# Optimization experiments

Measured on AMD Instinct MI355X. Metric: run time of the kernel, lower is better.

The kernel has to match this reference:

```python
import jax, jax.numpy as jnp
import numpy as np

BN_EPS = 1e-5


def trilinear_sample(feat, grid):
    """F.grid_sample 5D, mode='bilinear', padding_mode='border', align_corners=True.
    feat: (B,C,D,H,W); grid: (B,N,3) in [-1,1], last dim ordered (x,y,z) -> (W,H,D).
    Returns (B,N,C)."""
    B, C, D, H, W = feat.shape
    # align_corners=True unnormalization; border padding == clamp continuous coord
    x = jnp.clip((grid[..., 0] + 1.0) * 0.5 * (W - 1), 0.0, W - 1)
    y = jnp.clip((grid[..., 1] + 1.0) * 0.5 * (H - 1), 0.0, H - 1)
    z = jnp.clip((grid[..., 2] + 1.0) * 0.5 * (D - 1), 0.0, D - 1)
    x0 = jnp.floor(x).astype(jnp.int32); x1 = jnp.minimum(x0 + 1, W - 1)
    y0 = jnp.floor(y).astype(jnp.int32); y1 = jnp.minimum(y0 + 1, H - 1)
    z0 = jnp.floor(z).astype(jnp.int32); z1 = jnp.minimum(z0 + 1, D - 1)
    wx = (x - x0)[:, None, :]  # (B,1,N)
    wy = (y - y0)[:, None, :]
    wz = (z - z0)[:, None, :]
    flat = feat.reshape(B, C, D * H * W)

    def gather(zi, yi, xi):
        idx = (zi * H + yi) * W + xi            # (B,N)
        return jnp.take_along_axis(flat, idx[:, None, :], axis=2)  # (B,C,N)

    c00 = gather(z0, y0, x0) * (1 - wx) + gather(z0, y0, x1) * wx
    c01 = gather(z0, y1, x0) * (1 - wx) + gather(z0, y1, x1) * wx
    c10 = gather(z1, y0, x0) * (1 - wx) + gather(z1, y0, x1) * wx
    c11 = gather(z1, y1, x0) * (1 - wx) + gather(z1, y1, x1) * wx
    c0 = c00 * (1 - wy) + c01 * wy
    c1 = c10 * (1 - wy) + c11 * wy
    out = c0 * (1 - wz) + c1 * wz               # (B,C,N)
    return out.transpose(0, 2, 1)                # (B,N,C)


def batchnorm(x, gamma, beta, mean, var):
    # inference-mode BatchNorm1d over channel (last) dim
    return (x - mean) * jax.lax.rsqrt(var + BN_EPS) * gamma + beta


def setup_inputs() -> dict:
    key = jax.random.key(0)
    ks = jax.random.split(key, 16)
    B, C, D, H, W = 2, 128, 64, 64, 64
    N = 65536
    h1, h2 = 512, 512
    inp = {
        "dense_features": jax.random.normal(ks[0], (B, C, D, H, W), dtype=jnp.float32),
        "query_points": jax.random.uniform(ks[1], (B, N, 3), dtype=jnp.float32),
        "W1": jax.random.normal(ks[2], (C, h1), dtype=jnp.float32) / np.sqrt(C),
        "b1": jax.random.normal(ks[3], (h1,), dtype=jnp.float32) * 0.01,
        "g1": jax.random.uniform(ks[4], (h1,), dtype=jnp.float32, minval=0.5, maxval=1.5),
        "be1": jax.random.normal(ks[5], (h1,), dtype=jnp.float32) * 0.1,
        "m1": jax.random.normal(ks[6], (h1,), dtype=jnp.float32) * 0.1,
        "v1": jax.random.uniform(ks[7], (h1,), dtype=jnp.float32, minval=0.5, maxval=1.5),
        "W2": jax.random.normal(ks[8], (h1, h2), dtype=jnp.float32) / np.sqrt(h1),
        "b2": jax.random.normal(ks[9], (h2,), dtype=jnp.float32) * 0.01,
        "g2": jax.random.uniform(ks[10], (h2,), dtype=jnp.float32, minval=0.5, maxval=1.5),
        "be2": jax.random.normal(ks[11], (h2,), dtype=jnp.float32) * 0.1,
        "m2": jax.random.normal(ks[12], (h2,), dtype=jnp.float32) * 0.1,
        "v2": jax.random.uniform(ks[13], (h2,), dtype=jnp.float32, minval=0.5, maxval=1.5),
        "W3": jax.random.normal(ks[14], (h2, 1), dtype=jnp.float32) / np.sqrt(h2),
        "b3": jax.random.normal(ks[15], (1,), dtype=jnp.float32) * 0.01,
    }
    return inp


def reference(dense_features, query_points, W1, b1, g1, be1, m1, v1,
              W2, b2, g2, be2, m2, v2, W3, b3):
    grid = 2.0 * query_points - 1.0                       # (B,N,3)
    feats = trilinear_sample(dense_features, grid)        # (B,N,128)
    h = jax.nn.relu(batchnorm(jnp.einsum('bnc,ch->bnh', feats, W1) + b1, g1, be1, m1, v1))
    h = jax.nn.relu(batchnorm(jnp.einsum('bnc,ch->bnh', h, W2) + b2, g2, be2, m2, v2))
    out = jnp.einsum('bnc,ch->bnh', h, W3) + b3           # (B,N,1)
    return out
```

## Files before the change

kernel.cpp:

```cpp
#include <hip/hip_runtime.h>
#include <hip/hip_bf16.h>

using bf16x8 = __attribute__((ext_vector_type(8))) short;
using f32x4  = __attribute__((ext_vector_type(4))) float;
using u32x4  = __attribute__((ext_vector_type(4))) unsigned int;
typedef unsigned short u16;
typedef unsigned int u32;

#define NB    2
#define NC    128
#define NPTS  65536
#define MTOT  (NB*NPTS)
#define NTILE (MTOT/64)

static __device__ __forceinline__ u16 f2bf(float f) {
    u32 u = __float_as_uint(f);
    u32 r = (u + 0x7FFFu + ((u >> 16) & 1u)) >> 16;
    return (u16)r;
}
static __device__ __forceinline__ float bflo(u32 d) { return __uint_as_float(d << 16); }
static __device__ __forceinline__ float bfhi(u32 d) { return __uint_as_float(d & 0xFFFF0000u); }

__global__ void prep_kernel(
    const float* __restrict__ W1, const float* __restrict__ W2,
    const float* __restrict__ b1, const float* __restrict__ g1, const float* __restrict__ be1,
    const float* __restrict__ m1, const float* __restrict__ v1,
    const float* __restrict__ b2, const float* __restrict__ g2, const float* __restrict__ be2,
    const float* __restrict__ m2, const float* __restrict__ v2,
    u16* __restrict__ W1p, u16* __restrict__ W2p,
    float* __restrict__ s1, float* __restrict__ t1,
    float* __restrict__ s2, float* __restrict__ t2)
{
    int id = blockIdx.x * 256 + threadIdx.x;
    {
        int l = id & 63, nf = (id >> 6) & 3, kk = (id >> 8) & 15, w = id >> 12;
        int n  = w * 64 + nf * 16 + (l & 15);
        int c0 = kk * 32 + (l >> 4) * 8;
        #pragma unroll
        for (int j = 0; j < 8; ++j)
            W2p[id * 8 + j] = f2bf(W2[(size_t)(c0 + j) * 512 + n]);
    }
    if (id < 8192) {
        int l = id & 63, nf = (id >> 6) & 3, kk = (id >> 8) & 3, w = id >> 10;
        int n  = w * 64 + nf * 16 + (l & 15);
        int c0 = kk * 32 + (l >> 4) * 8;
        #pragma unroll
        for (int j = 0; j < 8; ++j)
            W1p[id * 8 + j] = f2bf(W1[(size_t)(c0 + j) * 512 + n]);
    }
    if (id < 512) {
        float s = g1[id] * rsqrtf(v1[id] + 1e-5f);
        s1[id] = s;
        t1[id] = (b1[id] - m1[id]) * s + be1[id];
        float ss = g2[id] * rsqrtf(v2[id] + 1e-5f);
        s2[id] = ss;
        t2[id] = (b2[id] - m2[id]) * ss + be2[id];
    }
}

__global__ __launch_bounds__(256) void transpose_kernel(const float* __restrict__ feat,
                                                        u16* __restrict__ featT)
{
    __shared__ float tile[128][33];
    int blk = blockIdx.x;
    int b   = blk >> 13;
    int v0  = (blk & 8191) << 5;
    int t   = threadIdx.x;
    const float* fb = feat + ((size_t)b << 25) + v0;
    int c_l = t >> 3, f4 = t & 7;
    #pragma unroll
    for (int r = 0; r < 4; ++r) {
        int c = c_l + 32 * r;
        float4 v = *(const float4*)(fb + ((size_t)c << 18) + f4 * 4);
        tile[c][f4 * 4 + 0] = v.x;
        tile[c][f4 * 4 + 1] = v.y;
        tile[c][f4 * 4 + 2] = v.z;
        tile[c][f4 * 4 + 3] = v.w;
    }
    __syncthreads();
    u32* outp = (u32*)(featT + (((size_t)b << 18) + v0) * 128);
    #pragma unroll
    for (int r = 0; r < 2; ++r) {
        int idx = t + 256 * r;
        int v   = idx >> 4;
        int c4  = idx & 15;
        u32x4 o;
        #pragma unroll
        for (int k = 0; k < 4; ++k) {
            float lo = tile[8 * c4 + 2 * k + 0][v];
            float hi = tile[8 * c4 + 2 * k + 1][v];
            o[k] = (u32)f2bf(lo) | ((u32)f2bf(hi) << 16);
        }
        *(u32x4*)(outp + (size_t)v * 64 + c4 * 4) = o;
    }
}

template<bool SAMP>
__global__ __launch_bounds__(512, 4) void fused_kernel(
    const u16* __restrict__ featT, const u16* __restrict__ feats,
    const float* __restrict__ qp,
    const u16* __restrict__ W1p, const u16* __restrict__ W2p,
    const float* __restrict__ s1, const float* __restrict__ t1,
    const float* __restrict__ s2, const float* __restrict__ t2,
    const float* __restrict__ W3, const float* __restrict__ b3,
    float* __restrict__ out)
{
    __shared__ u16 h1[64 * 512];
    __shared__ float outb[512];
    u16* atile = h1;

    const int tidx = threadIdx.x;
    const int w    = tidx >> 6;
    const int l    = tidx & 63;
    const int l15  = l & 15;
    const int lq   = l >> 4;
    const int m0   = blockIdx.x * 64;
    const int n0   = w * 64;

    const u16* B1 = W1p + (size_t)(w * 4)  * 4 * 512;
    const u16* B2 = W2p + (size_t)(w * 16) * 4 * 512;

#define LOADB1(dst, kk) { _Pragma("unroll") for (int nf = 0; nf < 4; ++nf) \
    (dst)[nf] = *(const bf16x8*)(B1 + ((kk) * 4 + nf) * 512 + l * 8); }
#define LOADB2(dst, kk) { _Pragma("unroll") for (int nf = 0; nf < 4; ++nf) \
    (dst)[nf] = *(const bf16x8*)(B2 + ((kk) * 4 + nf) * 512 + l * 8); }
#define LDSA(dst, kk) { _Pragma("unroll") for (int mf = 0; mf < 4; ++mf) { \
    int row = mf * 16 + l15; \
    (dst)[mf] = *(const bf16x8*)(atile + row * 128 + ((((kk) * 4 + lq) ^ (row & 7)) << 3)); } }
#define LOADA2(dst, kk) { _Pragma("unroll") for (int mf = 0; mf < 4; ++mf) { \
    int row = mf * 16 + l15; \
    (dst)[mf] = *(const bf16x8*)(h1 + row * 512 + (((kk) * 32 + lq * 8) ^ ((row & 7) << 3))); } }

    if (SAMP) {
        const int li = tidx & 15;
        const int pr = tidx >> 4;
        const int co = li * 4;
        #pragma unroll
        for (int half = 0; half < 2; ++half) {
            int row = pr + 32 * half;
            int p   = m0 + row;
            int b   = p >> 16;
            float qx = qp[p * 3 + 0], qy = qp[p * 3 + 1], qz = qp[p * 3 + 2];
            float x = fminf(fmaxf(qx * 63.0f, 0.0f), 63.0f);
            float y = fminf(fmaxf(qy * 63.0f, 0.0f), 63.0f);
            float z = fminf(fmaxf(qz * 63.0f, 0.0f), 63.0f);
            int x0 = (int)floorf(x), y0 = (int)floorf(y), z0 = (int)floorf(z);
            int x1 = min(x0 + 1, 63), y1 = min(y0 + 1, 63), z1 = min(z0 + 1, 63);
            float wx = x - (float)x0, wy = y - (float)y0, wz = z - (float)z0;
            const u32* fb = (const u32*)featT + ((size_t)b << 24);
            int zy00 = z0 * 4096 + y0 * 64, zy01 = z0 * 4096 + y1 * 64;
            int zy10 = z1 * 4096 + y0 * 64, zy11 = z1 * 4096 + y1 * 64;
            u32x4 d000 = *(const u32x4*)(fb + (size_t)(zy00 + x0) * 64 + co);
            u32x4 d001 = *(const u32x4*)(fb + (size_t)(zy00 + x1) * 64 + co);
            u32x4 d010 = *(const u32x4*)(fb + (size_t)(zy01 + x0) * 64 + co);
            u32x4 d011 = *(const u32x4*)(fb + (size_t)(zy01 + x1) * 64 + co);
            u32x4 d100 = *(const u32x4*)(fb + (size_t)(zy10 + x0) * 64 + co);
            u32x4 d101 = *(const u32x4*)(fb + (size_t)(zy10 + x1) * 64 + co);
            u32x4 d110 = *(const u32x4*)(fb + (size_t)(zy11 + x0) * 64 + co);
            u32x4 d111 = *(const u32x4*)(fb + (size_t)(zy11 + x1) * 64 + co);
            float omx = 1.0f - wx, omy = 1.0f - wy, omz = 1.0f - wz;
            u32x4 o;
            #pragma unroll
            for (int j = 0; j < 4; ++j) {
                float c00 = bflo(d000[j]) * omx + bflo(d001[j]) * wx;
                float c01 = bflo(d010[j]) * omx + bflo(d011[j]) * wx;
                float c10 = bflo(d100[j]) * omx + bflo(d101[j]) * wx;
                float c11 = bflo(d110[j]) * omx + bflo(d111[j]) * wx;
                float rl  = (c00 * omy + c01 * wy) * omz + (c10 * omy + c11 * wy) * wz;
                float e00 = bfhi(d000[j]) * omx + bfhi(d001[j]) * wx;
                float e01 = bfhi(d010[j]) * omx + bfhi(d011[j]) * wx;
                float e10 = bfhi(d100[j]) * omx + bfhi(d101[j]) * wx;
                float e11 = bfhi(d110[j]) * omx + bfhi(d111[j]) * wx;
                float rh  = (e00 * omy + e01 * wy) * omz + (e10 * omy + e11 * wy) * wz;
                o[j] = (u32)f2bf(rl) | ((u32)f2bf(rh) << 16);
            }
            *(u32x4*)(atile + row * 128 + ((li ^ (row & 7)) << 3)) = o;
        }
    } else {
        #pragma unroll
        for (int r2 = 0; r2 < 2; ++r2) {
            int idx = tidx + 512 * r2;
            int row = idx >> 4, ch = idx & 15;
            u32x4 v = *(const u32x4*)(feats + (size_t)(m0 + row) * 128 + ch * 8);
            *(u32x4*)(atile + row * 128 + ((ch ^ (row & 7)) << 3)) = v;
        }
    }
    __syncthreads();

    f32x4 acc[4][4];
    #pragma unroll
    for (int i = 0; i < 4; ++i)
        #pragma unroll
        for (int j = 0; j < 4; ++j) acc[i][j] = (f32x4){0.f, 0.f, 0.f, 0.f};
    {
        bf16x8 bv[2][4];
        LOADB1(bv[0], 0);
        #pragma unroll
        for (int kk = 0; kk < 4; ++kk) {
            const int cur = kk & 1, nxt = cur ^ 1;
            if (kk < 3) LOADB1(bv[nxt], kk + 1);
            bf16x8 av[4];
            LDSA(av, kk);
            __builtin_amdgcn_s_setprio(1);
            #pragma unroll
            for (int mf = 0; mf < 4; ++mf)
                #pragma unroll
                for (int nf = 0; nf < 4; ++nf)
                    acc[mf][nf] = __builtin_amdgcn_mfma_f32_16x16x32_bf16(av[mf], bv[cur][nf], acc[mf][nf], 0, 0, 0);
            __builtin_amdgcn_s_setprio(0);
        }
    }

    bf16x8 pb[2][4];
    LOADB2(pb[0], 0);
    __syncthreads();

    {
        float s1v[4], t1v[4];
        #pragma unroll
        for (int nf = 0; nf < 4; ++nf) {
            int col = n0 + nf * 16 + l15;
            s1v[nf] = s1[col]; t1v[nf] = t1[col];
        }
        #pragma unroll
        for (int mf = 0; mf < 4; ++mf)
            #pragma unroll
            for (int nf = 0; nf < 4; ++nf) {
                int col = n0 + nf * 16 + l15;
                #pragma unroll
                for (int i = 0; i < 4; ++i) {
                    int row = mf * 16 + lq * 4 + i;
                    float v = fmaxf(acc[mf][nf][i] * s1v[nf] + t1v[nf], 0.0f);
                    h1[row * 512 + (col ^ ((row & 7) << 3))] = f2bf(v);
                }
            }
    }
    __syncthreads();

    f32x4 acc2[4][4];
    #pragma unroll
    for (int i = 0; i < 4; ++i)
        #pragma unroll
        for (int j = 0; j < 4; ++j) acc2[i][j] = (f32x4){0.f, 0.f, 0.f, 0.f};
    {
        #pragma unroll
        for (int kk = 0; kk < 16; ++kk) {
            const int cur = kk & 1, nxt = cur ^ 1;
            if (kk < 15) LOADB2(pb[nxt], kk + 1);
            bf16x8 a2[4];
            LOADA2(a2, kk);
            __builtin_amdgcn_s_setprio(1);
            #pragma unroll
            for (int mf = 0; mf < 4; ++mf)
                #pragma unroll
                for (int nf = 0; nf < 4; ++nf)
                    acc2[mf][nf] = __builtin_amdgcn_mfma_f32_16x16x32_bf16(a2[mf], pb[cur][nf], acc2[mf][nf], 0, 0, 0);
            __builtin_amdgcn_s_setprio(0);
        }
    }

    float part[16];
    #pragma unroll
    for (int i = 0; i < 16; ++i) part[i] = 0.f;
    {
        float s2v[4], t2v[4], w3v[4];
        #pragma unroll
        for (int nf = 0; nf < 4; ++nf) {
            int col = n0 + nf * 16 + l15;
            s2v[nf] = s2[col]; t2v[nf] = t2[col]; w3v[nf] = W3[col];
        }
        #pragma unroll
        for (int mf = 0; mf < 4; ++mf)
            #pragma unroll
            for (int nf = 0; nf < 4; ++nf)
                #pragma unroll
                for (int i = 0; i < 4; ++i) {
                    float h = fmaxf(acc2[mf][nf][i] * s2v[nf] + t2v[nf], 0.0f);
                    part[mf * 4 + i] += h * w3v[nf];
                }
    }
    #pragma unroll
    for (int off = 1; off < 16; off <<= 1)
        #pragma unroll
        for (int i = 0; i < 16; ++i) part[i] += __shfl_xor(part[i], off, 64);

    if (l15 == 0) {
        #pragma unroll
        for (int mf = 0; mf < 4; ++mf)
            #pragma unroll
            for (int i = 0; i < 4; ++i)
                outb[w * 64 + mf * 16 + lq * 4 + i] = part[mf * 4 + i];
    }
    __syncthreads();
    if (tidx < 64) {
        float r = b3[0];
        #pragma unroll
        for (int ww = 0; ww < 8; ++ww) r += outb[ww * 64 + tidx];
        out[m0 + tidx] = r;
    }
#undef LOADB1
#undef LOADB2
#undef LDSA
#undef LOADA2
}

__global__ void sample_kernel(const float* __restrict__ feat,
                              const float* __restrict__ qp,
                              u16* __restrict__ fo)
{
    int tid = blockIdx.x * 256 + threadIdx.x;
    int p = tid >> 7;
    int c = tid & 127;
    int b = p >> 16;

    float qx = qp[p * 3 + 0], qy = qp[p * 3 + 1], qz = qp[p * 3 + 2];
    float x = fminf(fmaxf(qx * 63.0f, 0.0f), 63.0f);
    float y = fminf(fmaxf(qy * 63.0f, 0.0f), 63.0f);
    float z = fminf(fmaxf(qz * 63.0f, 0.0f), 63.0f);
    int x0 = (int)floorf(x), y0 = (int)floorf(y), z0 = (int)floorf(z);
    int x1 = min(x0 + 1, 63), y1 = min(y0 + 1, 63), z1 = min(z0 + 1, 63);
    float wx = x - (float)x0, wy = y - (float)y0, wz = z - (float)z0;

    const float* fb = feat + ((size_t)(b * NC + c) << 18);
    int zy00 = z0 * 4096 + y0 * 64, zy01 = z0 * 4096 + y1 * 64;
    int zy10 = z1 * 4096 + y0 * 64, zy11 = z1 * 4096 + y1 * 64;
    float f000 = fb[zy00 + x0], f001 = fb[zy00 + x1];
    float f010 = fb[zy01 + x0], f011 = fb[zy01 + x1];
    float f100 = fb[zy10 + x0], f101 = fb[zy10 + x1];
    float f110 = fb[zy11 + x0], f111 = fb[zy11 + x1];

    float omx = 1.0f - wx;
    float c00 = f000 * omx + f001 * wx;
    float c01 = f010 * omx + f011 * wx;
    float c10 = f100 * omx + f101 * wx;
    float c11 = f110 * omx + f111 * wx;
    float omy = 1.0f - wy;
    float c0 = c00 * omy + c01 * wy;
    float c1 = c10 * omy + c11 * wy;
    float v  = c0 * (1.0f - wz) + c1 * wz;
    fo[(size_t)p * 128 + c] = f2bf(v);
}

extern "C" void kernel_launch(void* const* d_in, const int* in_sizes, int n_in,
                              void* d_out, int out_size, void* d_ws, size_t ws_size,
                              hipStream_t stream)
{
    const float* feat = (const float*)d_in[0];
    const float* qp   = (const float*)d_in[1];
    const float* W1   = (const float*)d_in[2];
    const float* b1   = (const float*)d_in[3];
    const float* g1   = (const float*)d_in[4];
    const float* be1  = (const float*)d_in[5];
    const float* m1   = (const float*)d_in[6];
    const float* v1   = (const float*)d_in[7];
    const float* W2   = (const float*)d_in[8];
    const float* b2   = (const float*)d_in[9];
    const float* g2   = (const float*)d_in[10];
    const float* be2  = (const float*)d_in[11];
    const float* m2   = (const float*)d_in[12];
    const float* v2   = (const float*)d_in[13];
    const float* W3   = (const float*)d_in[14];
    const float* b3   = (const float*)d_in[15];

    char* ws = (char*)d_ws;
    u16*   W1p   = (u16*)(ws);
    u16*   W2p   = (u16*)(ws + 131072);
    float* s1    = (float*)(ws + 655360);
    float* t1    = (float*)(ws + 657408);
    float* s2    = (float*)(ws + 659456);
    float* t2    = (float*)(ws + 661504);
    u16*   feats = (u16*)(ws + 663552);
    u16*   featT = (u16*)(ws + 663552 + 33554432);
    const size_t needed = 663552 + 33554432 + 134217728;

    prep_kernel<<<128, 256, 0, stream>>>(W1, W2, b1, g1, be1, m1, v1,
                                         b2, g2, be2, m2, v2,
                                         W1p, W2p, s1, t1, s2, t2);
    if (ws_size >= needed) {
        transpose_kernel<<<16384, 256, 0, stream>>>(feat, featT);
        fused_kernel<true><<<NTILE, 512, 0, stream>>>(featT, feats, qp, W1p, W2p,
                                                      s1, t1, s2, t2, W3, b3, (float*)d_out);
    } else {
        sample_kernel<<<(MTOT * 128) / 256, 256, 0, stream>>>(feat, qp, feats);
        fused_kernel<false><<<NTILE, 512, 0, stream>>>(featT, feats, qp, W1p, W2p,
                                                       s1, t1, s2, t2, W3, b3, (float*)d_out);
    }
}
```

Measured before the change: 177.2 us.

## Double M tile to 128 rows with 1024-thread blocks and batched gather loads

```diff
diff --git a/kernel.cpp b/kernel.cpp
--- a/kernel.cpp
+++ b/kernel.cpp
@@ -11,7 +11,7 @@
 #define NC    128
 #define NPTS  65536
 #define MTOT  (NB*NPTS)
-#define NTILE (MTOT/64)
+#define NTILE2 (MTOT/128)
 
 static __device__ __forceinline__ u16 f2bf(float f) {
     u32 u = __float_as_uint(f);
@@ -96,7 +96,7 @@
 }
 
 template<bool SAMP>
-__global__ __launch_bounds__(512, 4) void fused_kernel(
+__global__ __launch_bounds__(1024, 4) void fused_kernel(
     const u16* __restrict__ featT, const u16* __restrict__ feats,
     const float* __restrict__ qp,
     const u16* __restrict__ W1p, const u16* __restrict__ W2p,
@@ -105,72 +105,84 @@
     const float* __restrict__ W3, const float* __restrict__ b3,
     float* __restrict__ out)
 {
-    __shared__ u16 h1[64 * 512];
-    __shared__ float outb[512];
+    __shared__ u16 h1[128 * 512];
+    __shared__ float outb[1024];
     u16* atile = h1;
 
     const int tidx = threadIdx.x;
     const int w    = tidx >> 6;
+    const int wr   = w >> 3;
+    const int wc   = w & 7;
     const int l    = tidx & 63;
     const int l15  = l & 15;
     const int lq   = l >> 4;
-    const int m0   = blockIdx.x * 64;
-    const int n0   = w * 64;
-
-    const u16* B1 = W1p + (size_t)(w * 4)  * 4 * 512;
-    const u16* B2 = W2p + (size_t)(w * 16) * 4 * 512;
+    const int m0   = blockIdx.x * 128;
+    const int mr0  = wr * 64;
+    const int n0   = wc * 64;
+
+    const u16* B1 = W1p + (size_t)(wc * 4)  * 4 * 512;
+    const u16* B2 = W2p + (size_t)(wc * 16) * 4 * 512;
 
 #define LOADB1(dst, kk) { _Pragma("unroll") for (int nf = 0; nf < 4; ++nf) \
     (dst)[nf] = *(const bf16x8*)(B1 + ((kk) * 4 + nf) * 512 + l * 8); }
 #define LOADB2(dst, kk) { _Pragma("unroll") for (int nf = 0; nf < 4; ++nf) \
     (dst)[nf] = *(const bf16x8*)(B2 + ((kk) * 4 + nf) * 512 + l * 8); }
 #define LDSA(dst, kk) { _Pragma("unroll") for (int mf = 0; mf < 4; ++mf) { \
-    int row = mf * 16 + l15; \
+    int row = mr0 + mf * 16 + l15; \
     (dst)[mf] = *(const bf16x8*)(atile + row * 128 + ((((kk) * 4 + lq) ^ (row & 7)) << 3)); } }
 #define LOADA2(dst, kk) { _Pragma("unroll") for (int mf = 0; mf < 4; ++mf) { \
-    int row = mf * 16 + l15; \
+    int row = mr0 + mf * 16 + l15; \
     (dst)[mf] = *(const bf16x8*)(h1 + row * 512 + (((kk) * 32 + lq * 8) ^ ((row & 7) << 3))); } }
 
     if (SAMP) {
         const int li = tidx & 15;
         const int pr = tidx >> 4;
         const int co = li * 4;
+        u32x4 d[2][8];
+        float wxh[2], wyh[2], wzh[2];
+        int rowh[2];
         #pragma unroll
         for (int half = 0; half < 2; ++half) {
-            int row = pr + 32 * half;
-            int p   = m0 + row;
-            int b   = p >> 16;
+            int row = pr + 64 * half;
+            rowh[half] = row;
+            int p = m0 + row;
+            int b = p >> 16;
             float qx = qp[p * 3 + 0], qy = qp[p * 3 + 1], qz = qp[p * 3 + 2];
             float x = fminf(fmaxf(qx * 63.0f, 0.0f), 63.0f);
             float y = fminf(fmaxf(qy * 63.0f, 0.0f), 63.0f);
             float z = fminf(fmaxf(qz * 63.0f, 0.0f), 63.0f);
             int x0 = (int)floorf(x), y0 = (int)floorf(y), z0 = (int)floorf(z);
             int x1 = min(x0 + 1, 63), y1 = min(y0 + 1, 63), z1 = min(z0 + 1, 63);
-            float wx = x - (float)x0, wy = y - (float)y0, wz = z - (float)z0;
+            wxh[half] = x - (float)x0; wyh[half] = y - (float)y0; wzh[half] = z - (float)z0;
             const u32* fb = (const u32*)featT + ((size_t)b << 24);
             int zy00 = z0 * 4096 + y0 * 64, zy01 = z0 * 4096 + y1 * 64;
             int zy10 = z1 * 4096 + y0 * 64, zy11 = z1 * 4096 + y1 * 64;
-            u32x4 d000 = *(const u32x4*)(fb + (size_t)(zy00 + x0) * 64 + co);
-            u32x4 d001 = *(const u32x4*)(fb + (size_t)(zy00 + x1) * 64 + co);
-            u32x4 d010 = *(const u32x4*)(fb + (size_t)(zy01 + x0) * 64 + co);
-            u32x4 d011 = *(const u32x4*)(fb + (size_t)(zy01 + x1) * 64 + co);
-            u32x4 d100 = *(const u32x4*)(fb + (size_t)(zy10 + x0) * 64 + co);
-            u32x4 d101 = *(const u32x4*)(fb + (size_t)(zy10 + x1) * 64 + co);
-            u32x4 d110 = *(const u32x4*)(fb + (size_t)(zy11 + x0) * 64 + co);
-            u32x4 d111 = *(const u32x4*)(fb + (size_t)(zy11 + x1) * 64 + co);
+            d[half][0] = *(const u32x4*)(fb + (size_t)(zy00 + x0) * 64 + co);
+            d[half][1] = *(const u32x4*)(fb + (size_t)(zy00 + x1) * 64 + co);
+            d[half][2] = *(const u32x4*)(fb + (size_t)(zy01 + x0) * 64 + co);
+            d[half][3] = *(const u32x4*)(fb + (size_t)(zy01 + x1) * 64 + co);
+            d[half][4] = *(const u32x4*)(fb + (size_t)(zy10 + x0) * 64 + co);
+            d[half][5] = *(const u32x4*)(fb + (size_t)(zy10 + x1) * 64 + co);
+            d[half][6] = *(const u32x4*)(fb + (size_t)(zy11 + x0) * 64 + co);
+            d[half][7] = *(const u32x4*)(fb + (size_t)(zy11 + x1) * 64 + co);
+        }
+        #pragma unroll
+        for (int half = 0; half < 2; ++half) {
+            float wx = wxh[half], wy = wyh[half], wz = wzh[half];
             float omx = 1.0f - wx, omy = 1.0f - wy, omz = 1.0f - wz;
+            int row = rowh[half];
             u32x4 o;
             #pragma unroll
             for (int j = 0; j < 4; ++j) {
-                float c00 = bflo(d000[j]) * omx + bflo(d001[j]) * wx;
-                float c01 = bflo(d010[j]) * omx + bflo(d011[j]) * wx;
-                float c10 = bflo(d100[j]) * omx + bflo(d101[j]) * wx;
-                float c11 = bflo(d110[j]) * omx + bflo(d111[j]) * wx;
+                float c00 = bflo(d[half][0][j]) * omx + bflo(d[half][1][j]) * wx;
+                float c01 = bflo(d[half][2][j]) * omx + bflo(d[half][3][j]) * wx;
+                float c10 = bflo(d[half][4][j]) * omx + bflo(d[half][5][j]) * wx;
+                float c11 = bflo(d[half][6][j]) * omx + bflo(d[half][7][j]) * wx;
                 float rl  = (c00 * omy + c01 * wy) * omz + (c10 * omy + c11 * wy) * wz;
-                float e00 = bfhi(d000[j]) * omx + bfhi(d001[j]) * wx;
-                float e01 = bfhi(d010[j]) * omx + bfhi(d011[j]) * wx;
-                float e10 = bfhi(d100[j]) * omx + bfhi(d101[j]) * wx;
-                float e11 = bfhi(d110[j]) * omx + bfhi(d111[j]) * wx;
+                float e00 = bfhi(d[half][0][j]) * omx + bfhi(d[half][1][j]) * wx;
+                float e01 = bfhi(d[half][2][j]) * omx + bfhi(d[half][3][j]) * wx;
+                float e10 = bfhi(d[half][4][j]) * omx + bfhi(d[half][5][j]) * wx;
+                float e11 = bfhi(d[half][6][j]) * omx + bfhi(d[half][7][j]) * wx;
                 float rh  = (e00 * omy + e01 * wy) * omz + (e10 * omy + e11 * wy) * wz;
                 o[j] = (u32)f2bf(rl) | ((u32)f2bf(rh) << 16);
             }
@@ -179,12 +191,15 @@
     } else {
         #pragma unroll
         for (int r2 = 0; r2 < 2; ++r2) {
-            int idx = tidx + 512 * r2;
+            int idx = tidx + 1024 * r2;
             int row = idx >> 4, ch = idx & 15;
             u32x4 v = *(const u32x4*)(feats + (size_t)(m0 + row) * 128 + ch * 8);
             *(u32x4*)(atile + row * 128 + ((ch ^ (row & 7)) << 3)) = v;
         }
     }
+
+    bf16x8 bv[2][4];
+    LOADB1(bv[0], 0);
     __syncthreads();
 
     f32x4 acc[4][4];
@@ -193,8 +208,6 @@
         #pragma unroll
         for (int j = 0; j < 4; ++j) acc[i][j] = (f32x4){0.f, 0.f, 0.f, 0.f};
     {
-        bf16x8 bv[2][4];
-        LOADB1(bv[0], 0);
         #pragma unroll
         for (int kk = 0; kk < 4; ++kk) {
             const int cur = kk & 1, nxt = cur ^ 1;
@@ -229,7 +242,7 @@
                 int col = n0 + nf * 16 + l15;
                 #pragma unroll
                 for (int i = 0; i < 4; ++i) {
-                    int row = mf * 16 + lq * 4 + i;
+                    int row = mr0 + mf * 16 + lq * 4 + i;
                     float v = fmaxf(acc[mf][nf][i] * s1v[nf] + t1v[nf], 0.0f);
                     h1[row * 512 + (col ^ ((row & 7) << 3))] = f2bf(v);
                 }
@@ -292,11 +305,12 @@
                 outb[w * 64 + mf * 16 + lq * 4 + i] = part[mf * 4 + i];
     }
     __syncthreads();
-    if (tidx < 64) {
-        float r = b3[0];
-        #pragma unroll
-        for (int ww = 0; ww < 8; ++ww) r += outb[ww * 64 + tidx];
-        out[m0 + tidx] = r;
+    if (tidx < 128) {
+        int r = tidx >> 6, m = tidx & 63;
+        float s = b3[0];
+        #pragma unroll
+        for (int c = 0; c < 8; ++c) s += outb[(r * 8 + c) * 64 + m];
+        out[m0 + tidx] = s;
     }
 #undef LOADB1
 #undef LOADB2
@@ -378,11 +392,11 @@
                                          W1p, W2p, s1, t1, s2, t2);
     if (ws_size >= needed) {
         transpose_kernel<<<16384, 256, 0, stream>>>(feat, featT);
-        fused_kernel<true><<<NTILE, 512, 0, stream>>>(featT, feats, qp, W1p, W2p,
-                                                      s1, t1, s2, t2, W3, b3, (float*)d_out);
+        fused_kernel<true><<<NTILE2, 1024, 0, stream>>>(featT, feats, qp, W1p, W2p,
+                                                        s1, t1, s2, t2, W3, b3, (float*)d_out);
     } else {
         sample_kernel<<<(MTOT * 128) / 256, 256, 0, stream>>>(feat, qp, feats);
-        fused_kernel<false><<<NTILE, 512, 0, stream>>>(featT, feats, qp, W1p, W2p,
-                                                       s1, t1, s2, t2, W3, b3, (float*)d_out);
-    }
-}
+        fused_kernel<false><<<NTILE2, 1024, 0, stream>>>(featT, feats, qp, W1p, W2p,
+                                                         s1, t1, s2, t2, W3, b3, (float*)d_out);
+    }
+}
```

Result: slower. 190.7 us (+7.6%).

## Merge weight prep into transpose launch and batch sampling gathers before interpolation

Applied to the files above, without the earlier changes.

```diff
diff --git a/kernel.cpp b/kernel.cpp
--- a/kernel.cpp
+++ b/kernel.cpp
@@ -20,6 +20,43 @@
 }
 static __device__ __forceinline__ float bflo(u32 d) { return __uint_as_float(d << 16); }
 static __device__ __forceinline__ float bfhi(u32 d) { return __uint_as_float(d & 0xFFFF0000u); }
+
+static __device__ __forceinline__ void prep_body(
+    int id,
+    const float* __restrict__ W1, const float* __restrict__ W2,
+    const float* __restrict__ b1, const float* __restrict__ g1, const float* __restrict__ be1,
+    const float* __restrict__ m1, const float* __restrict__ v1,
+    const float* __restrict__ b2, const float* __restrict__ g2, const float* __restrict__ be2,
+    const float* __restrict__ m2, const float* __restrict__ v2,
+    u16* __restrict__ W1p, u16* __restrict__ W2p,
+    float* __restrict__ s1, float* __restrict__ t1,
+    float* __restrict__ s2, float* __restrict__ t2)
+{
+    {
+        int l = id & 63, nf = (id >> 6) & 3, kk = (id >> 8) & 15, w = id >> 12;
+        int n  = w * 64 + nf * 16 + (l & 15);
+        int c0 = kk * 32 + (l >> 4) * 8;
+        #pragma unroll
+        for (int j = 0; j < 8; ++j)
+            W2p[id * 8 + j] = f2bf(W2[(size_t)(c0 + j) * 512 + n]);
+    }
+    if (id < 8192) {
+        int l = id & 63, nf = (id >> 6) & 3, kk = (id >> 8) & 3, w = id >> 10;
+        int n  = w * 64 + nf * 16 + (l & 15);
+        int c0 = kk * 32 + (l >> 4) * 8;
+        #pragma unroll
+        for (int j = 0; j < 8; ++j)
+            W1p[id * 8 + j] = f2bf(W1[(size_t)(c0 + j) * 512 + n]);
+    }
+    if (id < 512) {
+        float s = g1[id] * rsqrtf(v1[id] + 1e-5f);
+        s1[id] = s;
+        t1[id] = (b1[id] - m1[id]) * s + be1[id];
+        float ss = g2[id] * rsqrtf(v2[id] + 1e-5f);
+        s2[id] = ss;
+        t2[id] = (b2[id] - m2[id]) * ss + be2[id];
+    }
+}
 
 __global__ void prep_kernel(
     const float* __restrict__ W1, const float* __restrict__ W2,
@@ -31,38 +68,28 @@
     float* __restrict__ s1, float* __restrict__ t1,
     float* __restrict__ s2, float* __restrict__ t2)
 {
-    int id = blockIdx.x * 256 + threadIdx.x;
-    {
-        int l = id & 63, nf = (id >> 6) & 3, kk = (id >> 8) & 15, w = id >> 12;
-        int n  = w * 64 + nf * 16 + (l & 15);
-        int c0 = kk * 32 + (l >> 4) * 8;
-        #pragma unroll
-        for (int j = 0; j < 8; ++j)
-            W2p[id * 8 + j] = f2bf(W2[(size_t)(c0 + j) * 512 + n]);
-    }
-    if (id < 8192) {
-        int l = id & 63, nf = (id >> 6) & 3, kk = (id >> 8) & 3, w = id >> 10;
-        int n  = w * 64 + nf * 16 + (l & 15);
-        int c0 = kk * 32 + (l >> 4) * 8;
-        #pragma unroll
-        for (int j = 0; j < 8; ++j)
-            W1p[id * 8 + j] = f2bf(W1[(size_t)(c0 + j) * 512 + n]);
-    }
-    if (id < 512) {
-        float s = g1[id] * rsqrtf(v1[id] + 1e-5f);
-        s1[id] = s;
-        t1[id] = (b1[id] - m1[id]) * s + be1[id];
-        float ss = g2[id] * rsqrtf(v2[id] + 1e-5f);
-        s2[id] = ss;
-        t2[id] = (b2[id] - m2[id]) * ss + be2[id];
-    }
-}
-
-__global__ __launch_bounds__(256) void transpose_kernel(const float* __restrict__ feat,
-                                                        u16* __restrict__ featT)
+    prep_body(blockIdx.x * 256 + threadIdx.x, W1, W2, b1, g1, be1, m1, v1,
+              b2, g2, be2, m2, v2, W1p, W2p, s1, t1, s2, t2);
+}
+
+__global__ __launch_bounds__(256) void transpose_kernel(
+    const float* __restrict__ feat, u16* __restrict__ featT,
+    const float* __restrict__ W1, const float* __restrict__ W2,
+    const float* __restrict__ b1, const float* __restrict__ g1, const float* __restrict__ be1,
+    const float* __restrict__ m1, const float* __restrict__ v1,
+    const float* __restrict__ b2, const float* __restrict__ g2, const float* __restrict__ be2,
+    const float* __restrict__ m2, const float* __restrict__ v2,
+    u16* __restrict__ W1p, u16* __restrict__ W2p,
+    float* __restrict__ s1, float* __restrict__ t1,
+    float* __restrict__ s2, float* __restrict__ t2)
 {
     __shared__ float tile[128][33];
     int blk = blockIdx.x;
+    if (blk >= 16384) {
+        prep_body((blk - 16384) * 256 + threadIdx.x, W1, W2, b1, g1, be1, m1, v1,
+                  b2, g2, be2, m2, v2, W1p, W2p, s1, t1, s2, t2);
+        return;
+    }
     int b   = blk >> 13;
     int v0  = (blk & 8191) << 5;
     int t   = threadIdx.x;
@@ -135,6 +162,8 @@
         const int li = tidx & 15;
         const int pr = tidx >> 4;
         const int co = li * 4;
+        u32x4 d[2][8];
+        float wxh[2], wyh[2], wzh[2];
         #pragma unroll
         for (int half = 0; half < 2; ++half) {
             int row = pr + 32 * half;
@@ -146,31 +175,36 @@
             float z = fminf(fmaxf(qz * 63.0f, 0.0f), 63.0f);
             int x0 = (int)floorf(x), y0 = (int)floorf(y), z0 = (int)floorf(z);
             int x1 = min(x0 + 1, 63), y1 = min(y0 + 1, 63), z1 = min(z0 + 1, 63);
-            float wx = x - (float)x0, wy = y - (float)y0, wz = z - (float)z0;
+            wxh[half] = x - (float)x0; wyh[half] = y - (float)y0; wzh[half] = z - (float)z0;
             const u32* fb = (const u32*)featT + ((size_t)b << 24);
             int zy00 = z0 * 4096 + y0 * 64, zy01 = z0 * 4096 + y1 * 64;
             int zy10 = z1 * 4096 + y0 * 64, zy11 = z1 * 4096 + y1 * 64;
-            u32x4 d000 = *(const u32x4*)(fb + (size_t)(zy00 + x0) * 64 + co);
-            u32x4 d001 = *(const u32x4*)(fb + (size_t)(zy00 + x1) * 64 + co);
-            u32x4 d010 = *(const u32x4*)(fb + (size_t)(zy01 + x0) * 64 + co);
-            u32x4 d011 = *(const u32x4*)(fb + (size_t)(zy01 + x1) * 64 + co);
-            u32x4 d100 = *(const u32x4*)(fb + (size_t)(zy10 + x0) * 64 + co);
-            u32x4 d101 = *(const u32x4*)(fb + (size_t)(zy10 + x1) * 64 + co);
-            u32x4 d110 = *(const u32x4*)(fb + (size_t)(zy11 + x0) * 64 + co);
-            u32x4 d111 = *(const u32x4*)(fb + (size_t)(zy11 + x1) * 64 + co);
+            d[half][0] = *(const u32x4*)(fb + (size_t)(zy00 + x0) * 64 + co);
+            d[half][1] = *(const u32x4*)(fb + (size_t)(zy00 + x1) * 64 + co);
+            d[half][2] = *(const u32x4*)(fb + (size_t)(zy01 + x0) * 64 + co);
+            d[half][3] = *(const u32x4*)(fb + (size_t)(zy01 + x1) * 64 + co);
+            d[half][4] = *(const u32x4*)(fb + (size_t)(zy10 + x0) * 64 + co);
+            d[half][5] = *(const u32x4*)(fb + (size_t)(zy10 + x1) * 64 + co);
+            d[half][6] = *(const u32x4*)(fb + (size_t)(zy11 + x0) * 64 + co);
+            d[half][7] = *(const u32x4*)(fb + (size_t)(zy11 + x1) * 64 + co);
+        }
+        #pragma unroll
+        for (int half = 0; half < 2; ++half) {
+            float wx = wxh[half], wy = wyh[half], wz = wzh[half];
             float omx = 1.0f - wx, omy = 1.0f - wy, omz = 1.0f - wz;
+            int row = pr + 32 * half;
             u32x4 o;
             #pragma unroll
             for (int j = 0; j < 4; ++j) {
-                float c00 = bflo(d000[j]) * omx + bflo(d001[j]) * wx;
-                float c01 = bflo(d010[j]) * omx + bflo(d011[j]) * wx;
-                float c10 = bflo(d100[j]) * omx + bflo(d101[j]) * wx;
-                float c11 = bflo(d110[j]) * omx + bflo(d111[j]) * wx;
+                float c00 = bflo(d[half][0][j]) * omx + bflo(d[half][1][j]) * wx;
+                float c01 = bflo(d[half][2][j]) * omx + bflo(d[half][3][j]) * wx;
+                float c10 = bflo(d[half][4][j]) * omx + bflo(d[half][5][j]) * wx;
+                float c11 = bflo(d[half][6][j]) * omx + bflo(d[half][7][j]) * wx;
                 float rl  = (c00 * omy + c01 * wy) * omz + (c10 * omy + c11 * wy) * wz;
-                float e00 = bfhi(d000[j]) * omx + bfhi(d001[j]) * wx;
-                float e01 = bfhi(d010[j]) * omx + bfhi(d011[j]) * wx;
-                float e10 = bfhi(d100[j]) * omx + bfhi(d101[j]) * wx;
-                float e11 = bfhi(d110[j]) * omx + bfhi(d111[j]) * wx;
+                float e00 = bfhi(d[half][0][j]) * omx + bfhi(d[half][1][j]) * wx;
+                float e01 = bfhi(d[half][2][j]) * omx + bfhi(d[half][3][j]) * wx;
+                float e10 = bfhi(d[half][4][j]) * omx + bfhi(d[half][5][j]) * wx;
+                float e11 = bfhi(d[half][6][j]) * omx + bfhi(d[half][7][j]) * wx;
                 float rh  = (e00 * omy + e01 * wy) * omz + (e10 * omy + e11 * wy) * wz;
                 o[j] = (u32)f2bf(rl) | ((u32)f2bf(rh) << 16);
             }
@@ -185,6 +219,9 @@
             *(u32x4*)(atile + row * 128 + ((ch ^ (row & 7)) << 3)) = v;
         }
     }
+
+    bf16x8 bv[2][4];
+    LOADB1(bv[0], 0);
     __syncthreads();
 
     f32x4 acc[4][4];
@@ -192,13 +229,13 @@
     for (int i = 0; i < 4; ++i)
         #pragma unroll
         for (int j = 0; j < 4; ++j) acc[i][j] = (f32x4){0.f, 0.f, 0.f, 0.f};
+    bf16x8 pb[2][4];
     {
-        bf16x8 bv[2][4];
-        LOADB1(bv[0], 0);
         #pragma unroll
         for (int kk = 0; kk < 4; ++kk) {
             const int cur = kk & 1, nxt = cur ^ 1;
             if (kk < 3) LOADB1(bv[nxt], kk + 1);
+            if (kk == 3) LOADB2(pb[0], 0);
             bf16x8 av[4];
             LDSA(av, kk);
             __builtin_amdgcn_s_setprio(1);
@@ -210,9 +247,6 @@
             __builtin_amdgcn_s_setprio(0);
         }
     }
-
-    bf16x8 pb[2][4];
-    LOADB2(pb[0], 0);
     __syncthreads();
 
     {
@@ -373,14 +407,16 @@
     u16*   featT = (u16*)(ws + 663552 + 33554432);
     const size_t needed = 663552 + 33554432 + 134217728;
 
-    prep_kernel<<<128, 256, 0, stream>>>(W1, W2, b1, g1, be1, m1, v1,
-                                         b2, g2, be2, m2, v2,
-                                         W1p, W2p, s1, t1, s2, t2);
     if (ws_size >= needed) {
-        transpose_kernel<<<16384, 256, 0, stream>>>(feat, featT);
+        transpose_kernel<<<16384 + 128, 256, 0, stream>>>(
+            feat, featT, W1, W2, b1, g1, be1, m1, v1, b2, g2, be2, m2, v2,
+            W1p, W2p, s1, t1, s2, t2);
         fused_kernel<true><<<NTILE, 512, 0, stream>>>(featT, feats, qp, W1p, W2p,
                                                       s1, t1, s2, t2, W3, b3, (float*)d_out);
     } else {
+        prep_kernel<<<128, 256, 0, stream>>>(W1, W2, b1, g1, be1, m1, v1,
+                                             b2, g2, be2, m2, v2,
+                                             W1p, W2p, s1, t1, s2, t2);
         sample_kernel<<<(MTOT * 128) / 256, 256, 0, stream>>>(feat, qp, feats);
         fused_kernel<false><<<NTILE, 512, 0, stream>>>(featT, feats, qp, W1p, W2p,
                                                        s1, t1, s2, t2, W3, b3, (float*)d_out);
```

Result: slower. 192.1 us (+8.4%).

## Double fused MLP tile to 128 rows and fold weight prep into transpose

Applied to the files above, without the earlier changes.

```diff
diff --git a/kernel.cpp b/kernel.cpp
--- a/kernel.cpp
+++ b/kernel.cpp
@@ -11,7 +11,7 @@
 #define NC    128
 #define NPTS  65536
 #define MTOT  (NB*NPTS)
-#define NTILE (MTOT/64)
+#define NTILE2 (MTOT/128)
 
 static __device__ __forceinline__ u16 f2bf(float f) {
     u32 u = __float_as_uint(f);
@@ -20,6 +20,43 @@
 }
 static __device__ __forceinline__ float bflo(u32 d) { return __uint_as_float(d << 16); }
 static __device__ __forceinline__ float bfhi(u32 d) { return __uint_as_float(d & 0xFFFF0000u); }
+
+static __device__ __forceinline__ void prep_body(
+    int id,
+    const float* __restrict__ W1, const float* __restrict__ W2,
+    const float* __restrict__ b1, const float* __restrict__ g1, const float* __restrict__ be1,
+    const float* __restrict__ m1, const float* __restrict__ v1,
+    const float* __restrict__ b2, const float* __restrict__ g2, const float* __restrict__ be2,
+    const float* __restrict__ m2, const float* __restrict__ v2,
+    u16* __restrict__ W1p, u16* __restrict__ W2p,
+    float* __restrict__ s1, float* __restrict__ t1,
+    float* __restrict__ s2, float* __restrict__ t2)
+{
+    {
+        int l = id & 63, nf = (id >> 6) & 3, kk = (id >> 8) & 15, w = id >> 12;
+        int n  = w * 64 + nf * 16 + (l & 15);
+        int c0 = kk * 32 + (l >> 4) * 8;
+        #pragma unroll
+        for (int j = 0; j < 8; ++j)
+            W2p[id * 8 + j] = f2bf(W2[(size_t)(c0 + j) * 512 + n]);
+    }
+    if (id < 8192) {
+        int l = id & 63, nf = (id >> 6) & 3, kk = (id >> 8) & 3, w = id >> 10;
+        int n  = w * 64 + nf * 16 + (l & 15);
+        int c0 = kk * 32 + (l >> 4) * 8;
+        #pragma unroll
+        for (int j = 0; j < 8; ++j)
+            W1p[id * 8 + j] = f2bf(W1[(size_t)(c0 + j) * 512 + n]);
+    }
+    if (id < 512) {
+        float s = g1[id] * rsqrtf(v1[id] + 1e-5f);
+        s1[id] = s;
+        t1[id] = (b1[id] - m1[id]) * s + be1[id];
+        float ss = g2[id] * rsqrtf(v2[id] + 1e-5f);
+        s2[id] = ss;
+        t2[id] = (b2[id] - m2[id]) * ss + be2[id];
+    }
+}
 
 __global__ void prep_kernel(
     const float* __restrict__ W1, const float* __restrict__ W2,
@@ -31,38 +68,28 @@
     float* __restrict__ s1, float* __restrict__ t1,
     float* __restrict__ s2, float* __restrict__ t2)
 {
-    int id = blockIdx.x * 256 + threadIdx.x;
-    {
-        int l = id & 63, nf = (id >> 6) & 3, kk = (id >> 8) & 15, w = id >> 12;
-        int n  = w * 64 + nf * 16 + (l & 15);
-        int c0 = kk * 32 + (l >> 4) * 8;
-        #pragma unroll
-        for (int j = 0; j < 8; ++j)
-            W2p[id * 8 + j] = f2bf(W2[(size_t)(c0 + j) * 512 + n]);
-    }
-    if (id < 8192) {
-        int l = id & 63, nf = (id >> 6) & 3, kk = (id >> 8) & 3, w = id >> 10;
-        int n  = w * 64 + nf * 16 + (l & 15);
-        int c0 = kk * 32 + (l >> 4) * 8;
-        #pragma unroll
-        for (int j = 0; j < 8; ++j)
-            W1p[id * 8 + j] = f2bf(W1[(size_t)(c0 + j) * 512 + n]);
-    }
-    if (id < 512) {
-        float s = g1[id] * rsqrtf(v1[id] + 1e-5f);
-        s1[id] = s;
-        t1[id] = (b1[id] - m1[id]) * s + be1[id];
-        float ss = g2[id] * rsqrtf(v2[id] + 1e-5f);
-        s2[id] = ss;
-        t2[id] = (b2[id] - m2[id]) * ss + be2[id];
-    }
-}
-
-__global__ __launch_bounds__(256) void transpose_kernel(const float* __restrict__ feat,
-                                                        u16* __restrict__ featT)
+    prep_body(blockIdx.x * 256 + threadIdx.x, W1, W2, b1, g1, be1, m1, v1,
+              b2, g2, be2, m2, v2, W1p, W2p, s1, t1, s2, t2);
+}
+
+__global__ __launch_bounds__(256) void transpose_kernel(
+    const float* __restrict__ feat, u16* __restrict__ featT,
+    const float* __restrict__ W1, const float* __restrict__ W2,
+    const float* __restrict__ b1, const float* __restrict__ g1, const float* __restrict__ be1,
+    const float* __restrict__ m1, const float* __restrict__ v1,
+    const float* __restrict__ b2, const float* __restrict__ g2, const float* __restrict__ be2,
+    const float* __restrict__ m2, const float* __restrict__ v2,
+    u16* __restrict__ W1p, u16* __restrict__ W2p,
+    float* __restrict__ s1, float* __restrict__ t1,
+    float* __restrict__ s2, float* __restrict__ t2)
 {
     __shared__ float tile[128][33];
     int blk = blockIdx.x;
+    if (blk >= 16384) {
+        prep_body((blk - 16384) * 256 + threadIdx.x, W1, W2, b1, g1, be1, m1, v1,
+                  b2, g2, be2, m2, v2, W1p, W2p, s1, t1, s2, t2);
+        return;
+    }
     int b   = blk >> 13;
     int v0  = (blk & 8191) << 5;
     int t   = threadIdx.x;
@@ -96,7 +123,7 @@
 }
 
 template<bool SAMP>
-__global__ __launch_bounds__(512, 4) void fused_kernel(
+__global__ __launch_bounds__(1024, 4) void fused_kernel(
     const u16* __restrict__ featT, const u16* __restrict__ feats,
     const float* __restrict__ qp,
     const u16* __restrict__ W1p, const u16* __restrict__ W2p,
@@ -105,30 +132,33 @@
     const float* __restrict__ W3, const float* __restrict__ b3,
     float* __restrict__ out)
 {
-    __shared__ u16 h1[64 * 512];
-    __shared__ float outb[512];
+    __shared__ u16 h1[128 * 512];
+    __shared__ float outb[1024];
     u16* atile = h1;
 
     const int tidx = threadIdx.x;
     const int w    = tidx >> 6;
+    const int wr   = w >> 3;
+    const int wc   = w & 7;
     const int l    = tidx & 63;
     const int l15  = l & 15;
     const int lq   = l >> 4;
-    const int m0   = blockIdx.x * 64;
-    const int n0   = w * 64;
-
-    const u16* B1 = W1p + (size_t)(w * 4)  * 4 * 512;
-    const u16* B2 = W2p + (size_t)(w * 16) * 4 * 512;
+    const int m0   = blockIdx.x * 128;
+    const int mr0  = wr * 64;
+    const int n0   = wc * 64;
+
+    const u16* B1 = W1p + (size_t)(wc * 4)  * 4 * 512;
+    const u16* B2 = W2p + (size_t)(wc * 16) * 4 * 512;
 
 #define LOADB1(dst, kk) { _Pragma("unroll") for (int nf = 0; nf < 4; ++nf) \
     (dst)[nf] = *(const bf16x8*)(B1 + ((kk) * 4 + nf) * 512 + l * 8); }
 #define LOADB2(dst, kk) { _Pragma("unroll") for (int nf = 0; nf < 4; ++nf) \
     (dst)[nf] = *(const bf16x8*)(B2 + ((kk) * 4 + nf) * 512 + l * 8); }
 #define LDSA(dst, kk) { _Pragma("unroll") for (int mf = 0; mf < 4; ++mf) { \
-    int row = mf * 16 + l15; \
+    int row = mr0 + mf * 16 + l15; \
     (dst)[mf] = *(const bf16x8*)(atile + row * 128 + ((((kk) * 4 + lq) ^ (row & 7)) << 3)); } }
 #define LOADA2(dst, kk) { _Pragma("unroll") for (int mf = 0; mf < 4; ++mf) { \
-    int row = mf * 16 + l15; \
+    int row = mr0 + mf * 16 + l15; \
     (dst)[mf] = *(const bf16x8*)(h1 + row * 512 + (((kk) * 32 + lq * 8) ^ ((row & 7) << 3))); } }
 
     if (SAMP) {
@@ -137,7 +167,7 @@
         const int co = li * 4;
         #pragma unroll
         for (int half = 0; half < 2; ++half) {
-            int row = pr + 32 * half;
+            int row = pr + 64 * half;
             int p   = m0 + row;
             int b   = p >> 16;
             float qx = qp[p * 3 + 0], qy = qp[p * 3 + 1], qz = qp[p * 3 + 2];
@@ -158,6 +188,7 @@
             u32x4 d101 = *(const u32x4*)(fb + (size_t)(zy10 + x1) * 64 + co);
             u32x4 d110 = *(const u32x4*)(fb + (size_t)(zy11 + x0) * 64 + co);
             u32x4 d111 = *(const u32x4*)(fb + (size_t)(zy11 + x1) * 64 + co);
+
             float omx = 1.0f - wx, omy = 1.0f - wy, omz = 1.0f - wz;
             u32x4 o;
             #pragma unroll
@@ -179,12 +210,15 @@
     } else {
         #pragma unroll
         for (int r2 = 0; r2 < 2; ++r2) {
-            int idx = tidx + 512 * r2;
+            int idx = tidx + 1024 * r2;
             int row = idx >> 4, ch = idx & 15;
             u32x4 v = *(const u32x4*)(feats + (size_t)(m0 + row) * 128 + ch * 8);
             *(u32x4*)(atile + row * 128 + ((ch ^ (row & 7)) << 3)) = v;
         }
     }
+
+    bf16x8 bv[2][4];
+    LOADB1(bv[0], 0);
     __syncthreads();
 
     f32x4 acc[4][4];
@@ -193,8 +227,6 @@
         #pragma unroll
         for (int j = 0; j < 4; ++j) acc[i][j] = (f32x4){0.f, 0.f, 0.f, 0.f};
     {
-        bf16x8 bv[2][4];
-        LOADB1(bv[0], 0);
         #pragma unroll
         for (int kk = 0; kk < 4; ++kk) {
             const int cur = kk & 1, nxt = cur ^ 1;
@@ -229,7 +261,7 @@
                 int col = n0 + nf * 16 + l15;
                 #pragma unroll
                 for (int i = 0; i < 4; ++i) {
-                    int row = mf * 16 + lq * 4 + i;
+                    int row = mr0 + mf * 16 + lq * 4 + i;
                     float v = fmaxf(acc[mf][nf][i] * s1v[nf] + t1v[nf], 0.0f);
                     h1[row * 512 + (col ^ ((row & 7) << 3))] = f2bf(v);
                 }
@@ -292,11 +324,12 @@
                 outb[w * 64 + mf * 16 + lq * 4 + i] = part[mf * 4 + i];
     }
     __syncthreads();
-    if (tidx < 64) {
-        float r = b3[0];
-        #pragma unroll
-        for (int ww = 0; ww < 8; ++ww) r += outb[ww * 64 + tidx];
-        out[m0 + tidx] = r;
+    if (tidx < 128) {
+        int r = tidx >> 6, m = tidx & 63;
+        float s = b3[0];
+        #pragma unroll
+        for (int c = 0; c < 8; ++c) s += outb[(r * 8 + c) * 64 + m];
+        out[m0 + tidx] = s;
     }
 #undef LOADB1
 #undef LOADB2
@@ -373,16 +406,18 @@
     u16*   featT = (u16*)(ws + 663552 + 33554432);
     const size_t needed = 663552 + 33554432 + 134217728;
 
-    prep_kernel<<<128, 256, 0, stream>>>(W1, W2, b1, g1, be1, m1, v1,
-                                         b2, g2, be2, m2, v2,
-                                         W1p, W2p, s1, t1, s2, t2);
     if (ws_size >= needed) {
-        transpose_kernel<<<16384, 256, 0, stream>>>(feat, featT);
-        fused_kernel<true><<<NTILE, 512, 0, stream>>>(featT, feats, qp, W1p, W2p,
-                                                      s1, t1, s2, t2, W3, b3, (float*)d_out);
+        transpose_kernel<<<16384 + 128, 256, 0, stream>>>(
+            feat, featT, W1, W2, b1, g1, be1, m1, v1, b2, g2, be2, m2, v2,
+            W1p, W2p, s1, t1, s2, t2);
+        fused_kernel<true><<<NTILE2, 1024, 0, stream>>>(featT, feats, qp, W1p, W2p,
+                                                        s1, t1, s2, t2, W3, b3, (float*)d_out);
     } else {
+        prep_kernel<<<128, 256, 0, stream>>>(W1, W2, b1, g1, be1, m1, v1,
+                                             b2, g2, be2, m2, v2,
+                                             W1p, W2p, s1, t1, s2, t2);
         sample_kernel<<<(MTOT * 128) / 256, 256, 0, stream>>>(feat, qp, feats);
-        fused_kernel<false><<<NTILE, 512, 0, stream>>>(featT, feats, qp, W1p, W2p,
-                                                       s1, t1, s2, t2, W3, b3, (float*)d_out);
-    }
-}
+        fused_kernel<false><<<NTILE2, 1024, 0, stream>>>(featT, feats, qp, W1p, W2p,
+                                                         s1, t1, s2, t2, W3, b3, (float*)d_out);
+    }
+}
```

Result: slower. 189.1 us (+6.7%).
